# Kernel tuning notes

Measured on AMD Instinct MI355X. Metric: run time of the kernel, lower is better.

The kernel has to match this reference:

```python
import jax, jax.numpy as jnp
import numpy as np

N = 100000      # num POIs (nodes)
M = 20000       # num trajectories (hyperedges)
NNZ = 1000000   # incidence entries
D = 128         # emb_dim
NUM_LAYERS = 3
NEG_SLOPE = 0.2  # PyG HypergraphConv leaky_relu default


def setup_inputs() -> dict:
    key = jax.random.key(0)
    ks = jax.random.split(key, 8)
    pois_embs = jax.random.normal(ks[0], (N, D), jnp.float32)
    traj_embs = jax.random.normal(ks[1], (M, D), jnp.float32)
    hyperedge_weight = jax.random.uniform(ks[2], (M,), jnp.float32)
    node_idx = jax.random.randint(ks[3], (NNZ,), 0, N, jnp.int32)
    edge_idx = jax.random.randint(ks[4], (NNZ,), 0, M, jnp.int32)
    # learned params of the shared HypergraphConv layer (heads=1, concat)
    W_lin = jax.random.normal(ks[5], (D, D), jnp.float32) / np.sqrt(D).astype(np.float32)
    att = jax.random.normal(ks[6], (2 * D,), jnp.float32) * 0.1
    bias = jnp.zeros((D,), jnp.float32)
    return dict(pois_embs=pois_embs, traj_embs=traj_embs,
                hyperedge_weight=hyperedge_weight,
                node_idx=node_idx, edge_idx=edge_idx,
                W_lin=W_lin, att=att, bias=bias)


def _segment_softmax(scores, seg, num_seg):
    smax = jax.ops.segment_max(scores, seg, num_segments=num_seg)
    smax = jnp.where(jnp.isfinite(smax), smax, 0.0)  # guard empty segments
    ex = jnp.exp(scores - smax[seg])
    den = jax.ops.segment_sum(ex, seg, num_segments=num_seg)
    return ex / (den[seg] + 1e-16)


def _hconv(x, traj_embs, hyperedge_weight, node_idx, edge_idx, W_lin, att, bias):
    # x: [N, D] node feats; traj_embs: [M, D] hyperedge feats
    xt = x @ W_lin            # [N, D]  lin(x)
    et = traj_embs @ W_lin    # [M, D]  lin(hyperedge_attr)
    # attention logits per incidence pair (additive decomposition of cat*att)
    s_n = xt @ att[:D]        # [N]
    s_e = et @ att[D:]        # [M]
    alpha = jax.nn.leaky_relu(s_n[node_idx] + s_e[edge_idx], NEG_SLOPE)  # [NNZ]
    alpha = _segment_softmax(alpha, node_idx, N)  # softmax grouped by node
    # degree normalizations: D = sum_e H_ve * w_e, B = |e|
    Ddeg = jax.ops.segment_sum(hyperedge_weight[edge_idx], node_idx, num_segments=N)
    Dinv = jnp.where(Ddeg > 0, 1.0 / Ddeg, 0.0)
    Bdeg = jax.ops.segment_sum(jnp.ones((NNZ,), xt.dtype), edge_idx, num_segments=M)
    Binv = jnp.where(Bdeg > 0, 1.0 / Bdeg, 0.0)
    # node -> edge: B^{-1} H^T (alpha * x)
    msg1 = (alpha * Binv[edge_idx])[:, None] * xt[node_idx]        # [NNZ, D]
    edge_out = jax.ops.segment_sum(msg1, edge_idx, num_segments=M)  # [M, D]
    # edge -> node: D^{-1} H (alpha * edge_out)
    msg2 = (alpha * Dinv[node_idx])[:, None] * edge_out[edge_idx]   # [NNZ, D]
    out = jax.ops.segment_sum(msg2, node_idx, num_segments=N)       # [N, D]
    return out + bias


def reference(pois_embs, traj_embs, hyperedge_weight, node_idx, edge_idx, W_lin, att, bias):
    cur = pois_embs
    acc = pois_embs  # running sum of stacked layer outputs (incl. input)
    for _ in range(NUM_LAYERS):
        cur = _hconv(cur, traj_embs, hyperedge_weight, node_idx, edge_idx, W_lin, att, bias) + cur
        acc = acc + cur
    return acc / jnp.asarray(NUM_LAYERS + 1, acc.dtype)  # mean over stack
```

## Files before the change

kernel.cpp:

```cpp
#include <hip/hip_runtime.h>
#include <cstdint>
#include <cstddef>

#define DIM 128
#define NEG_SLOPE 0.2f

#define EREP 16
#define NREP 8

typedef __attribute__((ext_vector_type(8))) short short8v;
typedef __attribute__((ext_vector_type(4))) float float4v;

__device__ __forceinline__ float bf_lo(uint u) { return __uint_as_float(u << 16); }
__device__ __forceinline__ float bf_hi(uint u) { return __uint_as_float(u & 0xffff0000u); }
__device__ __forceinline__ uint f2bf(float f) {
  uint u = __float_as_uint(f);
  return (u + 0x7fffu + ((u >> 16) & 1u)) >> 16;
}
__device__ __forceinline__ uint pack_bf2(float lo, float hi) {
  return f2bf(lo) | (f2bf(hi) << 16);
}
__device__ __forceinline__ float lrelu(float x) {
  return x >= 0.0f ? x : NEG_SLOPE * x;
}

__global__ void wswz_kernel(const float* __restrict__ W, ushort* __restrict__ Wswz)
{
  int i = blockIdx.x * 256 + threadIdx.x;
  int j = i & 7, lane = (i >> 3) & 63, nt = (i >> 9) & 7, kt = i >> 12;
  int k = kt * 32 + (lane >> 4) * 8 + j;
  int col = nt * 16 + (lane & 15);
  Wswz[i] = (ushort)f2bf(W[k * 128 + col]);
}

__global__ void poisbf_kernel(const float* __restrict__ pois,
                              uint4* __restrict__ pois_bf, int N_, int NP)
{
  int i = blockIdx.x * 256 + threadIdx.x;
  if (i >= NP * 16) return;
  int row = i >> 4;
  uint4 o;
  if (row < N_) {
    const float* src = pois + (size_t)i * 8;
    float4 f0 = *(const float4*)src;
    float4 f1 = *(const float4*)(src + 4);
    o.x = pack_bf2(f0.x, f0.y); o.y = pack_bf2(f0.z, f0.w);
    o.z = pack_bf2(f1.x, f1.y); o.w = pack_bf2(f1.z, f1.w);
  } else { o.x = o.y = o.z = o.w = 0; }
  pois_bf[i] = o;
}

__global__ __launch_bounds__(256) void gemm_mfma_kernel(
    const ushort* __restrict__ Xb, const ushort* __restrict__ Wswz,
    const float* __restrict__ att, ushort* __restrict__ Yb,
    float* __restrict__ s_n, int rowsN)
{
  __shared__ ushort st[64 * 128];
  int tid = threadIdx.x;
  int w = tid >> 6, lane = tid & 63;
  int q = lane >> 4, c = lane & 15;
  int r0b = blockIdx.x * 64;
  int r0 = r0b + w * 16;
  float4v acc[8];
#pragma unroll
  for (int nt = 0; nt < 8; ++nt) acc[nt] = (float4v){0.f, 0.f, 0.f, 0.f};
  const ushort* arow = Xb + (size_t)(r0 + c) * DIM + q * 8;
#pragma unroll
  for (int kt = 0; kt < 4; ++kt) {
    short8v a = *(const short8v*)(arow + kt * 32);
#pragma unroll
    for (int nt = 0; nt < 8; ++nt) {
      short8v b = *(const short8v*)(Wswz + ((((kt << 3) + nt) << 9) + (lane << 3)));
      acc[nt] = __builtin_amdgcn_mfma_f32_16x16x32_bf16(a, b, acc[nt], 0, 0, 0);
    }
  }
  float av[8];
#pragma unroll
  for (int nt = 0; nt < 8; ++nt) av[nt] = att[nt * 16 + c];
  float p0 = 0, p1 = 0, p2 = 0, p3 = 0;
#pragma unroll
  for (int nt = 0; nt < 8; ++nt) {
    p0 = fmaf(acc[nt][0], av[nt], p0);
    p1 = fmaf(acc[nt][1], av[nt], p1);
    p2 = fmaf(acc[nt][2], av[nt], p2);
    p3 = fmaf(acc[nt][3], av[nt], p3);
  }
#pragma unroll
  for (int m = 8; m >= 1; m >>= 1) {
    p0 += __shfl_xor(p0, m, 64);
    p1 += __shfl_xor(p1, m, 64);
    p2 += __shfl_xor(p2, m, 64);
    p3 += __shfl_xor(p3, m, 64);
  }
  if (c == 0) {
    int rb = r0 + q * 4;
    if (rb + 0 < rowsN) s_n[rb + 0] = p0;
    if (rb + 1 < rowsN) s_n[rb + 1] = p1;
    if (rb + 2 < rowsN) s_n[rb + 2] = p2;
    if (rb + 3 < rowsN) s_n[rb + 3] = p3;
  }
  ushort* sw = st + w * 2048;
#pragma unroll
  for (int nt = 0; nt < 8; ++nt) {
    sw[(q * 4 + 0) * 128 + nt * 16 + c] = (ushort)f2bf(acc[nt][0]);
    sw[(q * 4 + 1) * 128 + nt * 16 + c] = (ushort)f2bf(acc[nt][1]);
    sw[(q * 4 + 2) * 128 + nt * 16 + c] = (ushort)f2bf(acc[nt][2]);
    sw[(q * 4 + 3) * 128 + nt * 16 + c] = (ushort)f2bf(acc[nt][3]);
  }
  __syncthreads();
#pragma unroll
  for (int it = 0; it < 4; ++it) {
    int idx = tid + it * 256;
    int row = idx >> 4, seg = idx & 15;
    *(uint4*)(Yb + (size_t)(r0b + row) * DIM + seg * 8) =
        *(const uint4*)&st[row * 128 + seg * 8];
  }
}

__global__ __launch_bounds__(256) void se_kernel(
    const float* __restrict__ traj, const float* __restrict__ W,
    const float* __restrict__ att, const float* __restrict__ hw,
    float* __restrict__ s_e, float2* __restrict__ se_hw, int M_)
{
  __shared__ float wv[128];
  int tid = threadIdx.x;
  if (tid < 128) {
    const float* wr = W + (size_t)tid * 128;
    float acc = 0.0f;
#pragma unroll 4
    for (int k = 0; k < 128; ++k) acc = fmaf(wr[k], att[DIM + k], acc);
    wv[tid] = acc;
  }
  __syncthreads();
  int e = blockIdx.x * 4 + (tid >> 6);
  int lane = tid & 63;
  if (e >= M_) return;
  const float* row = traj + (size_t)e * DIM;
  float v = row[lane] * wv[lane] + row[lane + 64] * wv[lane + 64];
#pragma unroll
  for (int d = 32; d > 0; d >>= 1) v += __shfl_down(v, d, 64);
  if (lane == 0) {
    s_e[e] = v;
    float2 g; g.x = v; g.y = hw[e];
    se_hw[e] = g;
  }
}

__global__ void hist_rank_kernel(const int* __restrict__ node_idx,
                                 const int* __restrict__ edge_idx,
                                 int* __restrict__ ncnt_r, int* __restrict__ ecnt_r,
                                 int* __restrict__ r_n, int* __restrict__ r_e,
                                 int nnz, int M_, int N_)
{
  int t = blockIdx.x * blockDim.x + threadIdx.x;
  int j = t * 2;
  if (j >= nnz) return;
  int* ec = ecnt_r + (size_t)(t & (EREP - 1)) * M_;
  int* nc = ncnt_r + (size_t)(t & (NREP - 1)) * N_;
  if (j + 2 <= nnz) {
    int2 e = *(const int2*)&edge_idx[j];
    int2 n = *(const int2*)&node_idx[j];
    int a0 = atomicAdd(&ec[e.x], 1);
    int a1 = atomicAdd(&ec[e.y], 1);
    int b0 = atomicAdd(&nc[n.x], 1);
    int b1 = atomicAdd(&nc[n.y], 1);
    *(int2*)&r_e[j] = make_int2(a0, a1);
    *(int2*)&r_n[j] = make_int2(b0, b1);
  } else {
    r_e[j] = atomicAdd(&ec[edge_idx[j]], 1);
    r_n[j] = atomicAdd(&nc[node_idx[j]], 1);
  }
}

__global__ void repsum_kernel(int* __restrict__ cnt_r, int* __restrict__ cnt,
                              int nbins, int reps)
{
  int b = blockIdx.x * blockDim.x + threadIdx.x;
  if (b >= nbins) return;
  int s = 0;
  for (int r = 0; r < reps; ++r) {
    size_t o = (size_t)r * nbins + b;
    int v = cnt_r[o];
    cnt_r[o] = s;
    s += v;
  }
  cnt[b] = s;
}

__global__ __launch_bounds__(1024) void scan_block_kernel(
    const int* __restrict__ cnt, int* __restrict__ off,
    int* __restrict__ partials, int nbins)
{
  __shared__ int ws[16];
  int tid = threadIdx.x, lane = tid & 63, wid = tid >> 6;
  int base = blockIdx.x * 4096 + tid * 4;
  int x0 = base + 0 < nbins ? cnt[base + 0] : 0;
  int x1 = base + 1 < nbins ? cnt[base + 1] : 0;
  int x2 = base + 2 < nbins ? cnt[base + 2] : 0;
  int x3 = base + 3 < nbins ? cnt[base + 3] : 0;
  int t = x0 + x1 + x2 + x3;
  int v = t;
#pragma unroll
  for (int d = 1; d < 64; d <<= 1) {
    int y = __shfl_up(v, d, 64);
    if (lane >= d) v += y;
  }
  if (lane == 63) ws[wid] = v;
  __syncthreads();
  if (tid < 16) {
    int s = ws[tid];
#pragma unroll
    for (int d = 1; d < 16; d <<= 1) {
      int y = __shfl_up(s, d, 16);
      if (tid >= d) s += y;
    }
    ws[tid] = s;
  }
  __syncthreads();
  int pre = (wid > 0 ? ws[wid - 1] : 0) + (v - t);
  if (base + 0 < nbins) off[base + 0] = pre;
  if (base + 1 < nbins) off[base + 1] = pre + x0;
  if (base + 2 < nbins) off[base + 2] = pre + x0 + x1;
  if (base + 3 < nbins) off[base + 3] = pre + x0 + x1 + x2;
  if (tid == 0) partials[blockIdx.x] = ws[15];
}

__global__ __launch_bounds__(64) void scan_partials_kernel(
    int* __restrict__ partials, int nb)
{
  int lane = threadIdx.x;
  int t = lane < nb ? partials[lane] : 0;
  int v = t;
#pragma unroll
  for (int d = 1; d < 64; d <<= 1) {
    int y = __shfl_up(v, d, 64);
    if (lane >= d) v += y;
  }
  if (lane < nb) partials[lane] = v - t;
  if (lane == 63) partials[nb] = v;
}

__global__ void add_off_combine_kernel(int* __restrict__ off,
                                       const int* __restrict__ partials,
                                       int* __restrict__ pre,
                                       int nbins, int nb, int reps)
{
  int i = blockIdx.x * blockDim.x + threadIdx.x;
  if (i < nbins) {
    int o = off[i] + partials[i >> 12];
    off[i] = o;
    for (int r = 0; r < reps; ++r) pre[(size_t)r * nbins + i] += o;
  }
  if (i == 0) off[nbins] = partials[nb];
}

__global__ void scatter_edge_kernel(const int* __restrict__ node_idx,
                                    const int* __restrict__ edge_idx,
                                    const int* __restrict__ r_e,
                                    const int* __restrict__ pre_e,
                                    int* __restrict__ nd_e, int nnz, int M_)
{
  int j = (blockIdx.x * blockDim.x + threadIdx.x) * 4;
  if (j >= nnz) return;
  if (j + 4 <= nnz) {
    const int* p0 = pre_e + (size_t)((j >> 1) & (EREP - 1)) * M_;
    const int* p1 = pre_e + (size_t)(((j >> 1) + 1) & (EREP - 1)) * M_;
    int4 e = *(const int4*)&edge_idx[j];
    int4 n = *(const int4*)&node_idx[j];
    int4 re = *(const int4*)&r_e[j];
    nd_e[p0[e.x] + re.x] = n.x;
    nd_e[p0[e.y] + re.y] = n.y;
    nd_e[p1[e.z] + re.z] = n.z;
    nd_e[p1[e.w] + re.w] = n.w;
  } else {
    for (int k = j; k < nnz; ++k) {
      const int* pp = pre_e + (size_t)((k >> 1) & (EREP - 1)) * M_;
      nd_e[pp[edge_idx[k]] + r_e[k]] = node_idx[k];
    }
  }
}

__global__ void scatter_node_kernel(const int* __restrict__ node_idx,
                                    const int* __restrict__ edge_idx,
                                    const int* __restrict__ r_n,
                                    const int* __restrict__ pre_n,
                                    int* __restrict__ eidx_n, int nnz, int N_)
{
  int j = (blockIdx.x * blockDim.x + threadIdx.x) * 4;
  if (j >= nnz) return;
  if (j + 4 <= nnz) {
    const int* p0 = pre_n + (size_t)((j >> 1) & (NREP - 1)) * N_;
    const int* p1 = pre_n + (size_t)(((j >> 1) + 1) & (NREP - 1)) * N_;
    int4 e = *(const int4*)&edge_idx[j];
    int4 n = *(const int4*)&node_idx[j];
    int4 rn = *(const int4*)&r_n[j];
    eidx_n[p0[n.x] + rn.x] = e.x;
    eidx_n[p0[n.y] + rn.y] = e.y;
    eidx_n[p1[n.z] + rn.z] = e.z;
    eidx_n[p1[n.w] + rn.w] = e.w;
  } else {
    for (int k = j; k < nnz; ++k) {
      const int* pp = pre_n + (size_t)((k >> 1) & (NREP - 1)) * N_;
      eidx_n[pp[node_idx[k]] + r_n[k]] = edge_idx[k];
    }
  }
}

__global__ void softstat_kernel(const int* __restrict__ noff,
                                const int* __restrict__ eidx_n,
                                const float* __restrict__ s_n,
                                const float2* __restrict__ se_hw,
                                float2* __restrict__ ns2,
                                float* __restrict__ Dinv, int N_)
{
  int n = blockIdx.x * blockDim.x + threadIdx.x;
  if (n >= N_) return;
  int s = noff[n], e1 = noff[n + 1];
  float sn = s_n[n];
  float m = -INFINITY, den = 0.0f, d = 0.0f;
  int t = s;
  for (; t + 4 <= e1; t += 4) {
    int i0 = eidx_n[t], i1 = eidx_n[t + 1], i2 = eidx_n[t + 2], i3 = eidx_n[t + 3];
    float2 g0 = se_hw[i0], g1 = se_hw[i1], g2 = se_hw[i2], g3 = se_hw[i3];
    float l0 = lrelu(sn + g0.x), l1 = lrelu(sn + g1.x);
    float l2 = lrelu(sn + g2.x), l3 = lrelu(sn + g3.x);
    float mm = fmaxf(fmaxf(fmaxf(l0, l1), fmaxf(l2, l3)), m);
    den = den * __expf(m - mm) + __expf(l0 - mm) + __expf(l1 - mm)
        + __expf(l2 - mm) + __expf(l3 - mm);
    m = mm;
    d += g0.y + g1.y + g2.y + g3.y;
  }
  for (; t < e1; ++t) {
    float2 g = se_hw[eidx_n[t]];
    float l = lrelu(sn + g.x);
    float mm = fmaxf(l, m);
    den = den * __expf(m - mm) + __expf(l - mm);
    m = mm;
    d += g.y;
  }
  if (s == e1) m = 0.0f;
  float2 r;
  r.x = sn;
  r.y = m + __logf(den + 1e-16f);
  ns2[n] = r;
  Dinv[n] = d > 0.0f ? 1.0f / d : 0.0f;
}

__global__ __launch_bounds__(256) void msg1_kernel(
    const int* __restrict__ eoff, const int* __restrict__ nd_e,
    const float2* __restrict__ ns2, const float* __restrict__ s_e,
    const ushort* __restrict__ xt, uint* __restrict__ eo, int M_)
{
  int e = blockIdx.x * (blockDim.x >> 6) + (threadIdx.x >> 6);
  int lane = threadIdx.x & 63;
  if (e >= M_) return;
  int s = eoff[e], t1 = eoff[e + 1];
  int len = t1 - s;
  float binv = len > 0 ? 1.0f / (float)len : 0.0f;
  float se = s_e[e];
  const uint* xt4 = (const uint*)xt + lane;
  float2 acc = {0.0f, 0.0f};
  int t = s;
  for (; t + 8 <= t1; t += 8) {
    int n0 = nd_e[t],     n1 = nd_e[t + 1], n2 = nd_e[t + 2], n3 = nd_e[t + 3];
    int n4 = nd_e[t + 4], n5 = nd_e[t + 5], n6 = nd_e[t + 6], n7 = nd_e[t + 7];
    float2 q0 = ns2[n0], q1 = ns2[n1], q2 = ns2[n2], q3 = ns2[n3];
    float2 q4 = ns2[n4], q5 = ns2[n5], q6 = ns2[n6], q7 = ns2[n7];
    uint u0 = xt4[(size_t)n0 * 64], u1 = xt4[(size_t)n1 * 64];
    uint u2 = xt4[(size_t)n2 * 64], u3 = xt4[(size_t)n3 * 64];
    uint u4 = xt4[(size_t)n4 * 64], u5 = xt4[(size_t)n5 * 64];
    uint u6 = xt4[(size_t)n6 * 64], u7 = xt4[(size_t)n7 * 64];
    float c0 = __expf(lrelu(q0.x + se) - q0.y);
    float c1 = __expf(lrelu(q1.x + se) - q1.y);
    float c2 = __expf(lrelu(q2.x + se) - q2.y);
    float c3 = __expf(lrelu(q3.x + se) - q3.y);
    float c4 = __expf(lrelu(q4.x + se) - q4.y);
    float c5 = __expf(lrelu(q5.x + se) - q5.y);
    float c6 = __expf(lrelu(q6.x + se) - q6.y);
    float c7 = __expf(lrelu(q7.x + se) - q7.y);
    acc.x = fmaf(c0, bf_lo(u0), acc.x); acc.y = fmaf(c0, bf_hi(u0), acc.y);
    acc.x = fmaf(c1, bf_lo(u1), acc.x); acc.y = fmaf(c1, bf_hi(u1), acc.y);
    acc.x = fmaf(c2, bf_lo(u2), acc.x); acc.y = fmaf(c2, bf_hi(u2), acc.y);
    acc.x = fmaf(c3, bf_lo(u3), acc.x); acc.y = fmaf(c3, bf_hi(u3), acc.y);
    acc.x = fmaf(c4, bf_lo(u4), acc.x); acc.y = fmaf(c4, bf_hi(u4), acc.y);
    acc.x = fmaf(c5, bf_lo(u5), acc.x); acc.y = fmaf(c5, bf_hi(u5), acc.y);
    acc.x = fmaf(c6, bf_lo(u6), acc.x); acc.y = fmaf(c6, bf_hi(u6), acc.y);
    acc.x = fmaf(c7, bf_lo(u7), acc.x); acc.y = fmaf(c7, bf_hi(u7), acc.y);
  }
  for (; t < t1; ++t) {
    int nd = nd_e[t];
    float2 q = ns2[nd];
    uint u = xt4[(size_t)nd * 64];
    float c = __expf(lrelu(q.x + se) - q.y);
    acc.x = fmaf(c, bf_lo(u), acc.x);
    acc.y = fmaf(c, bf_hi(u), acc.y);
  }
  eo[(size_t)e * (DIM / 2) + lane] = pack_bf2(acc.x * binv, acc.y * binv);
}

__global__ __launch_bounds__(256) void msg2_kernel(
    const int* __restrict__ noff, const int* __restrict__ eidx_n,
    const float2* __restrict__ ns2, const float* __restrict__ Dinv,
    const float* __restrict__ s_e, const uint* __restrict__ eo,
    const float* __restrict__ bias,
    const float* __restrict__ cur_in,
    const float* __restrict__ x1, const float* __restrict__ x2,
    float* __restrict__ cur_out, uint* __restrict__ curbf_out,
    float* __restrict__ dout, int last, int N_)
{
  int n = blockIdx.x * (blockDim.x >> 6) + (threadIdx.x >> 6);
  int lane = threadIdx.x & 63;
  if (n >= N_) return;
  int s = noff[n], t1 = noff[n + 1];
  float2 nsv = ns2[n];
  float sn = nsv.x, lz = nsv.y;
  const uint* eo4 = eo + lane;
  float2 acc = {0.0f, 0.0f};
  int t = s;
  for (; t + 8 <= t1; t += 8) {
    int e0 = eidx_n[t],     e1 = eidx_n[t + 1], e2 = eidx_n[t + 2], e3 = eidx_n[t + 3];
    int e4 = eidx_n[t + 4], e5 = eidx_n[t + 5], e6 = eidx_n[t + 6], e7 = eidx_n[t + 7];
    float x0 = s_e[e0], xx1 = s_e[e1], xx2 = s_e[e2], x3 = s_e[e3];
    float x4 = s_e[e4], x5 = s_e[e5], x6 = s_e[e6], x7 = s_e[e7];
    uint u0 = eo4[(size_t)e0 * 64], u1 = eo4[(size_t)e1 * 64];
    uint u2 = eo4[(size_t)e2 * 64], u3 = eo4[(size_t)e3 * 64];
    uint u4 = eo4[(size_t)e4 * 64], u5 = eo4[(size_t)e5 * 64];
    uint u6 = eo4[(size_t)e6 * 64], u7 = eo4[(size_t)e7 * 64];
    float c0 = __expf(lrelu(sn + x0) - lz);
    float c1 = __expf(lrelu(sn + xx1) - lz);
    float c2 = __expf(lrelu(sn + xx2) - lz);
    float c3 = __expf(lrelu(sn + x3) - lz);
    float c4 = __expf(lrelu(sn + x4) - lz);
    float c5 = __expf(lrelu(sn + x5) - lz);
    float c6 = __expf(lrelu(sn + x6) - lz);
    float c7 = __expf(lrelu(sn + x7) - lz);
    acc.x = fmaf(c0, bf_lo(u0), acc.x); acc.y = fmaf(c0, bf_hi(u0), acc.y);
    acc.x = fmaf(c1, bf_lo(u1), acc.x); acc.y = fmaf(c1, bf_hi(u1), acc.y);
    acc.x = fmaf(c2, bf_lo(u2), acc.x); acc.y = fmaf(c2, bf_hi(u2), acc.y);
    acc.x = fmaf(c3, bf_lo(u3), acc.x); acc.y = fmaf(c3, bf_hi(u3), acc.y);
    acc.x = fmaf(c4, bf_lo(u4), acc.x); acc.y = fmaf(c4, bf_hi(u4), acc.y);
    acc.x = fmaf(c5, bf_lo(u5), acc.x); acc.y = fmaf(c5, bf_hi(u5), acc.y);
    acc.x = fmaf(c6, bf_lo(u6), acc.x); acc.y = fmaf(c6, bf_hi(u6), acc.y);
    acc.x = fmaf(c7, bf_lo(u7), acc.x); acc.y = fmaf(c7, bf_hi(u7), acc.y);
  }
  for (; t < t1; ++t) {
    int e = eidx_n[t];
    uint u = eo4[(size_t)e * 64];
    float c = __expf(lrelu(sn + s_e[e]) - lz);
    acc.x = fmaf(c, bf_lo(u), acc.x);
    acc.y = fmaf(c, bf_hi(u), acc.y);
  }
  float sc = Dinv[n];
  float2 b = ((const float2*)bias)[lane];
  size_t idx = (size_t)n * DIM + lane * 2;
  float cinx = cur_in[idx], ciny = cur_in[idx + 1];
  float cx = cinx + acc.x * sc + b.x;
  float cy = ciny + acc.y * sc + b.y;
  if (last) {
    dout[idx]     = (x1[idx]     + x2[idx]     + cinx + cx) * 0.25f;
    dout[idx + 1] = (x1[idx + 1] + x2[idx + 1] + ciny + cy) * 0.25f;
  } else {
    cur_out[idx] = cx; cur_out[idx + 1] = cy;
    curbf_out[(size_t)n * 64 + lane] = pack_bf2(cx, cy);
  }
}

static inline int cdiv(int a, int b) { return (a + b - 1) / b; }

extern "C" void kernel_launch(void* const* d_in, const int* in_sizes, int n_in,
                              void* d_out, int out_size, void* d_ws, size_t ws_size,
                              hipStream_t stream)
{
  const float* pois = (const float*)d_in[0];
  const float* traj = (const float*)d_in[1];
  const float* hw   = (const float*)d_in[2];
  const int* node_idx = (const int*)d_in[3];
  const int* edge_idx = (const int*)d_in[4];
  const float* W    = (const float*)d_in[5];
  const float* att  = (const float*)d_in[6];
  const float* bias = (const float*)d_in[7];
  float* dout = (float*)d_out;

  const int N   = in_sizes[0] / DIM;
  const int M   = in_sizes[2];
  const int NNZ = in_sizes[3];
  const int NP  = (N + 63) & ~63;

  char* p = (char*)d_ws;
  auto alloc = [&](size_t bytes) -> void* {
    void* r = (void*)p;
    p += (bytes + 255) & ~(size_t)255;
    return r;
  };
  ushort* xt_bf   = (ushort*)alloc((size_t)NP * DIM * 2);
  ushort* cur_bf  = (ushort*)alloc((size_t)NP * DIM * 2);
  ushort* pois_bf = (ushort*)alloc((size_t)NP * DIM * 2);
  ushort* W_swz   = (ushort*)alloc(16384 * 2);
  uint*   eo_bf = (uint*)alloc((size_t)M * (DIM / 2) * 4);
  float*  cur_a = (float*)alloc((size_t)N * DIM * 4);
  float*  cur_b = (float*)alloc((size_t)N * DIM * 4);
  float2* ns2   = (float2*)alloc((size_t)N * 8);
  float*  s_e  = (float*)alloc((size_t)M * 4);
  float2* se_hw = (float2*)alloc((size_t)M * 8);
  float*  s_n  = (float*)alloc((size_t)N * 4);
  float*  Dinv = (float*)alloc((size_t)N * 4);
  int* ecnt   = (int*)alloc((size_t)M * 4);
  int* ncnt   = (int*)alloc((size_t)N * 4);
  int* ecnt_r = (int*)alloc((size_t)EREP * M * 4);
  int* ncnt_r = (int*)alloc((size_t)NREP * N * 4);
  int* eoff = (int*)alloc((size_t)(M + 1) * 4);
  int* noff = (int*)alloc((size_t)(N + 1) * 4);
  int* r_e  = (int*)alloc((size_t)NNZ * 4);
  int* r_n  = (int*)alloc((size_t)NNZ * 4);
  int* nd_e   = (int*)alloc((size_t)NNZ * 4);
  int* eidx_n = (int*)alloc((size_t)NNZ * 4);
  int* part_e = (int*)alloc(65 * 4);
  int* part_n = (int*)alloc(65 * 4);
  (void)ws_size;

  const int nbE = cdiv(M, 4096), nbN = cdiv(N, 4096);

  hipMemsetAsync(ecnt_r, 0, (size_t)EREP * M * 4, stream);
  hipMemsetAsync(ncnt_r, 0, (size_t)NREP * N * 4, stream);
  hist_rank_kernel<<<cdiv(NNZ, 512), 256, 0, stream>>>(node_idx, edge_idx, ncnt_r, ecnt_r, r_n, r_e, NNZ, M, N);
  repsum_kernel<<<cdiv(M, 256), 256, 0, stream>>>(ecnt_r, ecnt, M, EREP);
  repsum_kernel<<<cdiv(N, 256), 256, 0, stream>>>(ncnt_r, ncnt, N, NREP);
  scan_block_kernel<<<nbE, 1024, 0, stream>>>(ecnt, eoff, part_e, M);
  scan_block_kernel<<<nbN, 1024, 0, stream>>>(ncnt, noff, part_n, N);
  scan_partials_kernel<<<1, 64, 0, stream>>>(part_e, nbE);
  scan_partials_kernel<<<1, 64, 0, stream>>>(part_n, nbN);
  add_off_combine_kernel<<<cdiv(M, 256), 256, 0, stream>>>(eoff, part_e, ecnt_r, M, nbE, EREP);
  add_off_combine_kernel<<<cdiv(N, 256), 256, 0, stream>>>(noff, part_n, ncnt_r, N, nbN, NREP);
  scatter_edge_kernel<<<cdiv(NNZ, 1024), 256, 0, stream>>>(node_idx, edge_idx, r_e, ecnt_r, nd_e, NNZ, M);
  scatter_node_kernel<<<cdiv(NNZ, 1024), 256, 0, stream>>>(node_idx, edge_idx, r_n, ncnt_r, eidx_n, NNZ, N);

  wswz_kernel<<<64, 256, 0, stream>>>(W, W_swz);
  se_kernel<<<cdiv(M, 4), 256, 0, stream>>>(traj, W, att, hw, s_e, se_hw, M);
  poisbf_kernel<<<cdiv(NP * 16, 256), 256, 0, stream>>>(pois, (uint4*)pois_bf, N, NP);

  for (int layer = 0; layer < 3; ++layer) {
    const ushort* gin = (layer == 0) ? pois_bf : cur_bf;
    gemm_mfma_kernel<<<NP / 64, 256, 0, stream>>>(gin, W_swz, att, xt_bf, s_n, N);
    softstat_kernel<<<cdiv(N, 256), 256, 0, stream>>>(noff, eidx_n, s_n, se_hw, ns2, Dinv, N);
    msg1_kernel<<<cdiv(M, 4), 256, 0, stream>>>(eoff, nd_e, ns2, s_e, xt_bf, eo_bf, M);
    const float* cin = (layer == 0) ? pois : (layer == 1 ? cur_a : cur_b);
    float* cout = (layer == 0) ? cur_a : cur_b;
    int last = (layer == 2) ? 1 : 0;
    msg2_kernel<<<cdiv(N, 4), 256, 0, stream>>>(noff, eidx_n, ns2, Dinv, s_e, eo_bf,
                                                bias, cin, pois, cur_a,
                                                cout, (uint*)cur_bf,
                                                dout, last, N);
  }
}
```

Measured before the change: 746.4 us.

## Switch intermediates from bf16 to fp16 and drop fp32 layer state buffers

Replaces bf16 storage and MFMA with fp16 throughout (weights, inputs, transformed features, edge outputs), and stores the per-layer residual state only as packed fp16 instead of both fp32 and bf16 copies. msg2 now reads the previous layer's state from the fp16 buffer and writes a single fp16 output, cutting fp32 read and write traffic for N x 128 per layer. This trades range for precision: fp16 can overflow on large values and carries the residual path at reduced precision.

Result: no change. 738.5 us (-1.1%).

```diff
diff --git a/kernel.cpp b/kernel.cpp
--- a/kernel.cpp
+++ b/kernel.cpp
@@ -1,6 +1,8 @@
 #include <hip/hip_runtime.h>
+#include <hip/hip_fp16.h>
 #include <cstdint>
 #include <cstddef>
+#include <cstring>
 
 #define DIM 128
 #define NEG_SLOPE 0.2f
@@ -8,17 +10,25 @@
 #define EREP 16
 #define NREP 8
 
-typedef __attribute__((ext_vector_type(8))) short short8v;
+typedef _Float16 half8v __attribute__((ext_vector_type(8)));
 typedef __attribute__((ext_vector_type(4))) float float4v;
 
-__device__ __forceinline__ float bf_lo(uint u) { return __uint_as_float(u << 16); }
-__device__ __forceinline__ float bf_hi(uint u) { return __uint_as_float(u & 0xffff0000u); }
-__device__ __forceinline__ uint f2bf(float f) {
-  uint u = __float_as_uint(f);
-  return (u + 0x7fffu + ((u >> 16) & 1u)) >> 16;
-}
-__device__ __forceinline__ uint pack_bf2(float lo, float hi) {
-  return f2bf(lo) | (f2bf(hi) << 16);
+__device__ __forceinline__ float2 h2f2(uint u) {
+  __half2 h;
+  __builtin_memcpy(&h, &u, 4);
+  return __half22float2(h);
+}
+__device__ __forceinline__ uint packh2(float lo, float hi) {
+  __half2 h = __floats2half2_rn(lo, hi);
+  uint u;
+  __builtin_memcpy(&u, &h, 4);
+  return u;
+}
+__device__ __forceinline__ ushort f2h_us(float f) {
+  __half h = __float2half_rn(f);
+  ushort us;
+  __builtin_memcpy(&us, &h, 2);
+  return us;
 }
 __device__ __forceinline__ float lrelu(float x) {
   return x >= 0.0f ? x : NEG_SLOPE * x;
@@ -30,11 +40,11 @@
   int j = i & 7, lane = (i >> 3) & 63, nt = (i >> 9) & 7, kt = i >> 12;
   int k = kt * 32 + (lane >> 4) * 8 + j;
   int col = nt * 16 + (lane & 15);
-  Wswz[i] = (ushort)f2bf(W[k * 128 + col]);
-}
-
-__global__ void poisbf_kernel(const float* __restrict__ pois,
-                              uint4* __restrict__ pois_bf, int N_, int NP)
+  Wswz[i] = f2h_us(W[k * 128 + col]);
+}
+
+__global__ void poish_kernel(const float* __restrict__ pois,
+                             uint4* __restrict__ pois_h, int N_, int NP)
 {
   int i = blockIdx.x * 256 + threadIdx.x;
   if (i >= NP * 16) return;
@@ -44,10 +54,10 @@
     const float* src = pois + (size_t)i * 8;
     float4 f0 = *(const float4*)src;
     float4 f1 = *(const float4*)(src + 4);
-    o.x = pack_bf2(f0.x, f0.y); o.y = pack_bf2(f0.z, f0.w);
-    o.z = pack_bf2(f1.x, f1.y); o.w = pack_bf2(f1.z, f1.w);
+    o.x = packh2(f0.x, f0.y); o.y = packh2(f0.z, f0.w);
+    o.z = packh2(f1.x, f1.y); o.w = packh2(f1.z, f1.w);
   } else { o.x = o.y = o.z = o.w = 0; }
-  pois_bf[i] = o;
+  pois_h[i] = o;
 }
 
 __global__ __launch_bounds__(256) void gemm_mfma_kernel(
@@ -67,11 +77,11 @@
   const ushort* arow = Xb + (size_t)(r0 + c) * DIM + q * 8;
 #pragma unroll
   for (int kt = 0; kt < 4; ++kt) {
-    short8v a = *(const short8v*)(arow + kt * 32);
+    half8v a = *(const half8v*)(arow + kt * 32);
 #pragma unroll
     for (int nt = 0; nt < 8; ++nt) {
-      short8v b = *(const short8v*)(Wswz + ((((kt << 3) + nt) << 9) + (lane << 3)));
-      acc[nt] = __builtin_amdgcn_mfma_f32_16x16x32_bf16(a, b, acc[nt], 0, 0, 0);
+      half8v b = *(const half8v*)(Wswz + ((((kt << 3) + nt) << 9) + (lane << 3)));
+      acc[nt] = __builtin_amdgcn_mfma_f32_16x16x32_f16(a, b, acc[nt], 0, 0, 0);
     }
   }
   float av[8];
@@ -102,10 +112,10 @@
   ushort* sw = st + w * 2048;
 #pragma unroll
   for (int nt = 0; nt < 8; ++nt) {
-    sw[(q * 4 + 0) * 128 + nt * 16 + c] = (ushort)f2bf(acc[nt][0]);
-    sw[(q * 4 + 1) * 128 + nt * 16 + c] = (ushort)f2bf(acc[nt][1]);
-    sw[(q * 4 + 2) * 128 + nt * 16 + c] = (ushort)f2bf(acc[nt][2]);
-    sw[(q * 4 + 3) * 128 + nt * 16 + c] = (ushort)f2bf(acc[nt][3]);
+    sw[(q * 4 + 0) * 128 + nt * 16 + c] = f2h_us(acc[nt][0]);
+    sw[(q * 4 + 1) * 128 + nt * 16 + c] = f2h_us(acc[nt][1]);
+    sw[(q * 4 + 2) * 128 + nt * 16 + c] = f2h_us(acc[nt][2]);
+    sw[(q * 4 + 3) * 128 + nt * 16 + c] = f2h_us(acc[nt][3]);
   }
   __syncthreads();
 #pragma unroll
@@ -378,24 +388,27 @@
     float c5 = __expf(lrelu(q5.x + se) - q5.y);
     float c6 = __expf(lrelu(q6.x + se) - q6.y);
     float c7 = __expf(lrelu(q7.x + se) - q7.y);
-    acc.x = fmaf(c0, bf_lo(u0), acc.x); acc.y = fmaf(c0, bf_hi(u0), acc.y);
-    acc.x = fmaf(c1, bf_lo(u1), acc.x); acc.y = fmaf(c1, bf_hi(u1), acc.y);
-    acc.x = fmaf(c2, bf_lo(u2), acc.x); acc.y = fmaf(c2, bf_hi(u2), acc.y);
-    acc.x = fmaf(c3, bf_lo(u3), acc.x); acc.y = fmaf(c3, bf_hi(u3), acc.y);
-    acc.x = fmaf(c4, bf_lo(u4), acc.x); acc.y = fmaf(c4, bf_hi(u4), acc.y);
-    acc.x = fmaf(c5, bf_lo(u5), acc.x); acc.y = fmaf(c5, bf_hi(u5), acc.y);
-    acc.x = fmaf(c6, bf_lo(u6), acc.x); acc.y = fmaf(c6, bf_hi(u6), acc.y);
-    acc.x = fmaf(c7, bf_lo(u7), acc.x); acc.y = fmaf(c7, bf_hi(u7), acc.y);
+    float2 f0 = h2f2(u0), f1 = h2f2(u1), f2 = h2f2(u2), f3 = h2f2(u3);
+    float2 f4 = h2f2(u4), f5 = h2f2(u5), f6 = h2f2(u6), f7 = h2f2(u7);
+    acc.x = fmaf(c0, f0.x, acc.x); acc.y = fmaf(c0, f0.y, acc.y);
+    acc.x = fmaf(c1, f1.x, acc.x); acc.y = fmaf(c1, f1.y, acc.y);
+    acc.x = fmaf(c2, f2.x, acc.x); acc.y = fmaf(c2, f2.y, acc.y);
+    acc.x = fmaf(c3, f3.x, acc.x); acc.y = fmaf(c3, f3.y, acc.y);
+    acc.x = fmaf(c4, f4.x, acc.x); acc.y = fmaf(c4, f4.y, acc.y);
+    acc.x = fmaf(c5, f5.x, acc.x); acc.y = fmaf(c5, f5.y, acc.y);
+    acc.x = fmaf(c6, f6.x, acc.x); acc.y = fmaf(c6, f6.y, acc.y);
+    acc.x = fmaf(c7, f7.x, acc.x); acc.y = fmaf(c7, f7.y, acc.y);
   }
   for (; t < t1; ++t) {
     int nd = nd_e[t];
     float2 q = ns2[nd];
     uint u = xt4[(size_t)nd * 64];
     float c = __expf(lrelu(q.x + se) - q.y);
-    acc.x = fmaf(c, bf_lo(u), acc.x);
-    acc.y = fmaf(c, bf_hi(u), acc.y);
-  }
-  eo[(size_t)e * (DIM / 2) + lane] = pack_bf2(acc.x * binv, acc.y * binv);
+    float2 f = h2f2(u);
+    acc.x = fmaf(c, f.x, acc.x);
+    acc.y = fmaf(c, f.y, acc.y);
+  }
+  eo[(size_t)e * (DIM / 2) + lane] = packh2(acc.x * binv, acc.y * binv);
 }
 
 __global__ __launch_bounds__(256) void msg2_kernel(
@@ -403,10 +416,10 @@
     const float2* __restrict__ ns2, const float* __restrict__ Dinv,
     const float* __restrict__ s_e, const uint* __restrict__ eo,
     const float* __restrict__ bias,
-    const float* __restrict__ cur_in,
-    const float* __restrict__ x1, const float* __restrict__ x2,
-    float* __restrict__ cur_out, uint* __restrict__ curbf_out,
-    float* __restrict__ dout, int last, int N_)
+    const float* __restrict__ cin_f, const uint* __restrict__ cin_h,
+    const float* __restrict__ x1f, const uint* __restrict__ x2h,
+    uint* __restrict__ couth, float* __restrict__ dout,
+    int mode, int N_)
 {
   int n = blockIdx.x * (blockDim.x >> 6) + (threadIdx.x >> 6);
   int lane = threadIdx.x & 63;
@@ -434,34 +447,43 @@
     float c5 = __expf(lrelu(sn + x5) - lz);
     float c6 = __expf(lrelu(sn + x6) - lz);
     float c7 = __expf(lrelu(sn + x7) - lz);
-    acc.x = fmaf(c0, bf_lo(u0), acc.x); acc.y = fmaf(c0, bf_hi(u0), acc.y);
-    acc.x = fmaf(c1, bf_lo(u1), acc.x); acc.y = fmaf(c1, bf_hi(u1), acc.y);
-    acc.x = fmaf(c2, bf_lo(u2), acc.x); acc.y = fmaf(c2, bf_hi(u2), acc.y);
-    acc.x = fmaf(c3, bf_lo(u3), acc.x); acc.y = fmaf(c3, bf_hi(u3), acc.y);
-    acc.x = fmaf(c4, bf_lo(u4), acc.x); acc.y = fmaf(c4, bf_hi(u4), acc.y);
-    acc.x = fmaf(c5, bf_lo(u5), acc.x); acc.y = fmaf(c5, bf_hi(u5), acc.y);
-    acc.x = fmaf(c6, bf_lo(u6), acc.x); acc.y = fmaf(c6, bf_hi(u6), acc.y);
-    acc.x = fmaf(c7, bf_lo(u7), acc.x); acc.y = fmaf(c7, bf_hi(u7), acc.y);
+    float2 f0 = h2f2(u0), f1 = h2f2(u1), f2 = h2f2(u2), f3 = h2f2(u3);
+    float2 f4 = h2f2(u4), f5 = h2f2(u5), f6 = h2f2(u6), f7 = h2f2(u7);
+    acc.x = fmaf(c0, f0.x, acc.x); acc.y = fmaf(c0, f0.y, acc.y);
+    acc.x = fmaf(c1, f1.x, acc.x); acc.y = fmaf(c1, f1.y, acc.y);
+    acc.x = fmaf(c2, f2.x, acc.x); acc.y = fmaf(c2, f2.y, acc.y);
+    acc.x = fmaf(c3, f3.x, acc.x); acc.y = fmaf(c3, f3.y, acc.y);
+    acc.x = fmaf(c4, f4.x, acc.x); acc.y = fmaf(c4, f4.y, acc.y);
+    acc.x = fmaf(c5, f5.x, acc.x); acc.y = fmaf(c5, f5.y, acc.y);
+    acc.x = fmaf(c6, f6.x, acc.x); acc.y = fmaf(c6, f6.y, acc.y);
+    acc.x = fmaf(c7, f7.x, acc.x); acc.y = fmaf(c7, f7.y, acc.y);
   }
   for (; t < t1; ++t) {
     int e = eidx_n[t];
     uint u = eo4[(size_t)e * 64];
     float c = __expf(lrelu(sn + s_e[e]) - lz);
-    acc.x = fmaf(c, bf_lo(u), acc.x);
-    acc.y = fmaf(c, bf_hi(u), acc.y);
+    float2 f = h2f2(u);
+    acc.x = fmaf(c, f.x, acc.x);
+    acc.y = fmaf(c, f.y, acc.y);
   }
   float sc = Dinv[n];
   float2 b = ((const float2*)bias)[lane];
   size_t idx = (size_t)n * DIM + lane * 2;
-  float cinx = cur_in[idx], ciny = cur_in[idx + 1];
+  float cinx, ciny;
+  if (mode == 0) {
+    cinx = cin_f[idx]; ciny = cin_f[idx + 1];
+  } else {
+    float2 f = h2f2(cin_h[(size_t)n * 64 + lane]);
+    cinx = f.x; ciny = f.y;
+  }
   float cx = cinx + acc.x * sc + b.x;
   float cy = ciny + acc.y * sc + b.y;
-  if (last) {
-    dout[idx]     = (x1[idx]     + x2[idx]     + cinx + cx) * 0.25f;
-    dout[idx + 1] = (x1[idx + 1] + x2[idx + 1] + ciny + cy) * 0.25f;
+  if (mode == 2) {
+    float2 f2v = h2f2(x2h[(size_t)n * 64 + lane]);
+    dout[idx]     = (x1f[idx]     + f2v.x + cinx + cx) * 0.25f;
+    dout[idx + 1] = (x1f[idx + 1] + f2v.y + ciny + cy) * 0.25f;
   } else {
-    cur_out[idx] = cx; cur_out[idx + 1] = cy;
-    curbf_out[(size_t)n * 64 + lane] = pack_bf2(cx, cy);
+    couth[(size_t)n * 64 + lane] = packh2(cx, cy);
   }
 }
 
@@ -492,13 +514,12 @@
     p += (bytes + 255) & ~(size_t)255;
     return r;
   };
-  ushort* xt_bf   = (ushort*)alloc((size_t)NP * DIM * 2);
-  ushort* cur_bf  = (ushort*)alloc((size_t)NP * DIM * 2);
-  ushort* pois_bf = (ushort*)alloc((size_t)NP * DIM * 2);
+  ushort* xt_h    = (ushort*)alloc((size_t)NP * DIM * 2);
+  ushort* pois_h  = (ushort*)alloc((size_t)NP * DIM * 2);
+  uint*   cura_h  = (uint*)alloc((size_t)NP * 64 * 4);
+  uint*   curb_h  = (uint*)alloc((size_t)NP * 64 * 4);
   ushort* W_swz   = (ushort*)alloc(16384 * 2);
-  uint*   eo_bf = (uint*)alloc((size_t)M * (DIM / 2) * 4);
-  float*  cur_a = (float*)alloc((size_t)N * DIM * 4);
-  float*  cur_b = (float*)alloc((size_t)N * DIM * 4);
+  uint*   eo_h  = (uint*)alloc((size_t)M * (DIM / 2) * 4);
   float2* ns2   = (float2*)alloc((size_t)N * 8);
   float*  s_e  = (float*)alloc((size_t)M * 4);
   float2* se_hw = (float2*)alloc((size_t)M * 8);
@@ -536,19 +557,19 @@
 
   wswz_kernel<<<64, 256, 0, stream>>>(W, W_swz);
   se_kernel<<<cdiv(M, 4), 256, 0, stream>>>(traj, W, att, hw, s_e, se_hw, M);
-  poisbf_kernel<<<cdiv(NP * 16, 256), 256, 0, stream>>>(pois, (uint4*)pois_bf, N, NP);
+  poish_kernel<<<cdiv(NP * 16, 256), 256, 0, stream>>>(pois, (uint4*)pois_h, N, NP);
 
   for (int layer = 0; layer < 3; ++layer) {
-    const ushort* gin = (layer == 0) ? pois_bf : cur_bf;
-    gemm_mfma_kernel<<<NP / 64, 256, 0, stream>>>(gin, W_swz, att, xt_bf, s_n, N);
+    const ushort* gin = (layer == 0) ? pois_h
+                       : (layer == 1) ? (const ushort*)cura_h
+                                      : (const ushort*)curb_h;
+    gemm_mfma_kernel<<<NP / 64, 256, 0, stream>>>(gin, W_swz, att, xt_h, s_n, N);
     softstat_kernel<<<cdiv(N, 256), 256, 0, stream>>>(noff, eidx_n, s_n, se_hw, ns2, Dinv, N);
-    msg1_kernel<<<cdiv(M, 4), 256, 0, stream>>>(eoff, nd_e, ns2, s_e, xt_bf, eo_bf, M);
-    const float* cin = (layer == 0) ? pois : (layer == 1 ? cur_a : cur_b);
-    float* cout = (layer == 0) ? cur_a : cur_b;
-    int last = (layer == 2) ? 1 : 0;
-    msg2_kernel<<<cdiv(N, 4), 256, 0, stream>>>(noff, eidx_n, ns2, Dinv, s_e, eo_bf,
-                                                bias, cin, pois, cur_a,
-                                                cout, (uint*)cur_bf,
-                                                dout, last, N);
-  }
-}
+    msg1_kernel<<<cdiv(M, 4), 256, 0, stream>>>(eoff, nd_e, ns2, s_e, xt_h, eo_h, M);
+    const uint* cin_h = (layer == 1) ? cura_h : curb_h;
+    uint* couth = (layer == 0) ? cura_h : curb_h;
+    msg2_kernel<<<cdiv(N, 4), 256, 0, stream>>>(noff, eidx_n, ns2, Dinv, s_e, eo_h,
+                                                bias, pois, cin_h, pois, cura_h,
+                                                couth, dout, layer, N);
+  }
+}
```
